# Kernel optimization log

Measured on AMD Instinct MI355X. Metric: run time of the kernel, lower is better.

Reference implementation:

```python
import jax, jax.numpy as jnp
import numpy as np

N = 50000
IN_C = 128
OUT_C = 64


def gcn_conv(x, edge_index, W, b):
    # PyG GCNConv: h = X W; add self-loops; symmetric norm D^-1/2 (A+I) D^-1/2; aggregate; + bias
    n = x.shape[0]
    h = x @ W  # [N, out]
    loop = jnp.arange(n, dtype=edge_index.dtype)
    row = jnp.concatenate([edge_index[0], loop])  # source
    col = jnp.concatenate([edge_index[1], loop])  # target
    deg = jax.ops.segment_sum(jnp.ones_like(col, dtype=h.dtype), col, num_segments=n)
    dinv = jnp.where(deg > 0, jax.lax.rsqrt(deg), 0.0)
    norm = dinv[row] * dinv[col]  # [E+N]
    msg = norm[:, None] * h[row]  # gather source features
    out = jax.ops.segment_sum(msg, col, num_segments=n)  # scatter to targets
    return out + b


def layer_norm(x, w, b, eps=1e-5):
    mu = jnp.mean(x, axis=-1, keepdims=True)
    var = jnp.mean((x - mu) ** 2, axis=-1, keepdims=True)
    return (x - mu) * jax.lax.rsqrt(var + eps) * w + b


def setup_inputs() -> dict:
    key = jax.random.key(0)
    ks = jax.random.split(key, 10)
    x = jax.random.normal(ks[0], (N, IN_C), dtype=jnp.float32)
    edge_index = jax.random.randint(ks[1], (2, 800000), 0, N, dtype=jnp.int64)
    s1 = 1.0 / np.sqrt(IN_C)
    s2 = 1.0 / np.sqrt(OUT_C)
    W1 = jax.random.uniform(ks[2], (IN_C, OUT_C), jnp.float32, -s1, s1)
    b1 = jnp.zeros((OUT_C,), jnp.float32)
    ln_w = jnp.ones((OUT_C,), jnp.float32)
    ln_b = jnp.zeros((OUT_C,), jnp.float32)
    W2 = jax.random.uniform(ks[3], (OUT_C, OUT_C), jnp.float32, -s2, s2)
    b2 = jnp.zeros((OUT_C,), jnp.float32)
    W3 = jax.random.uniform(ks[4], (OUT_C, 6), jnp.float32, -s2, s2)
    b3 = jax.random.uniform(ks[5], (6,), jnp.float32, -s2, s2)
    return {"x": x, "edge_index": edge_index, "W1": W1, "b1": b1,
            "ln_w": ln_w, "ln_b": ln_b, "W2": W2, "b2": b2, "W3": W3, "b3": b3}


def reference(x, edge_index, W1, b1, ln_w, ln_b, W2, b2, W3, b3):
    h = gcn_conv(x, edge_index, W1, b1)           # [N, 64]
    h = jax.nn.relu(layer_norm(h, ln_w, ln_b))    # [N, 64]
    out1 = gcn_conv(h, edge_index, W2, b2)        # [N, 64]
    out2 = jax.nn.sigmoid(h @ W3 + b3)            # [N, 6]
    return (out1, out2)
```

## Files before the change

### kernel.cpp

```cpp
#include <hip/hip_runtime.h>
#include <hip/hip_fp16.h>
#include <math.h>


#define ELLW 48

typedef _Float16 half8 __attribute__((ext_vector_type(8)));
typedef float f32x4 __attribute__((ext_vector_type(4)));

__global__ void k_setup(const float* __restrict__ W1, const float* __restrict__ W2,
                        const float* __restrict__ W3, _Float16* __restrict__ W1g,
                        _Float16* __restrict__ Bg, int* __restrict__ cnt, int n) {
    if (blockIdx.x >= 52) {
        int i = (blockIdx.x - 52) * 256 + threadIdx.x;
        if (i < n) cnt[i] = 0;
        return;
    }
    int idx = blockIdx.x * 256 + threadIdx.x;
    if (idx < 8192) {
        int j = idx & 7, L = (idx >> 3) & 63, s = (idx >> 9) & 3, t = idx >> 11;
        int k = s * 32 + (L >> 4) * 8 + j;
        int c = t * 16 + (L & 15);
        W1g[idx] = (_Float16)W1[k * 64 + c];
    } else if (idx < 8192 + 5120) {
        int i2 = idx - 8192;
        int j = i2 & 7, L = (i2 >> 3) & 63, s = (i2 >> 9) & 1, u = i2 >> 10;
        int k = s * 32 + (L >> 4) * 8 + j;
        int c = (L & 15);
        float v;
        if (u < 4) v = W2[k * 64 + u * 16 + c];
        else v = (c < 6) ? W3[k * 6 + c] : 0.f;
        Bg[i2] = (_Float16)v;
    }
}

__global__ __launch_bounds__(256) void k_scatter(
    const int* __restrict__ row, const int* __restrict__ col,
    int* __restrict__ cnt, int* __restrict__ ell, int E, int slice_sz) {
    int slice = blockIdx.x & 7;
    int lo = slice * slice_sz;
    int hi = lo + slice_sz;
    int nchunk = gridDim.x >> 3;
    int stride = nchunk * 256;
    int v0 = (blockIdx.x >> 3) * 256 + threadIdx.x;
    int nv = E >> 2;
    const int4* c4p = (const int4*)col;
    const int4* r4p = (const int4*)row;
    for (int v = v0; v < nv; v += stride) {
        int4 c4 = c4p[v];
        int4 r4 = r4p[v];
        if (c4.x >= lo && c4.x < hi) {
            int rk = atomicAdd(&cnt[c4.x], 1);
            if (rk < ELLW) ell[c4.x * ELLW + rk] = r4.x << 7;
        }
        if (c4.y >= lo && c4.y < hi) {
            int rk = atomicAdd(&cnt[c4.y], 1);
            if (rk < ELLW) ell[c4.y * ELLW + rk] = r4.y << 7;
        }
        if (c4.z >= lo && c4.z < hi) {
            int rk = atomicAdd(&cnt[c4.z], 1);
            if (rk < ELLW) ell[c4.z * ELLW + rk] = r4.z << 7;
        }
        if (c4.w >= lo && c4.w < hi) {
            int rk = atomicAdd(&cnt[c4.w], 1);
            if (rk < ELLW) ell[c4.w * ELLW + rk] = r4.w << 7;
        }
    }
    if ((blockIdx.x >> 3) == 0) {
        for (int e = (nv << 2) + threadIdx.x; e < E; e += 256) {
            int c = col[e];
            if (c >= lo && c < hi) {
                int rk = atomicAdd(&cnt[c], 1);
                if (rk < ELLW) ell[c * ELLW + rk] = row[e] << 7;
            }
        }
    }
}

__global__ __launch_bounds__(256, 4) void k_gemm1(
    const float* __restrict__ x, const _Float16* __restrict__ W1g,
    const int* __restrict__ cnt, uint* __restrict__ hs,
    uint* __restrict__ h2s, int n) {
    int tid = threadIdx.x;
    if (blockIdx.x == 0) {
        if (tid < 32) hs[(size_t)n * 32 + tid] = 0u;
        else if (tid < 64) h2s[(size_t)n * 32 + (tid - 32)] = 0u;
    }
    int lane = tid & 63, wid = tid >> 6;
    int m16 = lane & 15, quad = lane >> 4;
    int node0 = blockIdx.x * 64 + wid * 16;
    int arow = node0 + m16;
    if (arow >= n) arow = n - 1;
    const float* xr = x + (size_t)arow * 128;
    half8 A[4];
#pragma unroll
    for (int s = 0; s < 4; s++) {
        const float4* p = (const float4*)(xr + s * 32 + quad * 8);
        float4 f0 = p[0], f1 = p[1];
        half8 a;
        a[0] = (_Float16)f0.x; a[1] = (_Float16)f0.y;
        a[2] = (_Float16)f0.z; a[3] = (_Float16)f0.w;
        a[4] = (_Float16)f1.x; a[5] = (_Float16)f1.y;
        a[6] = (_Float16)f1.z; a[7] = (_Float16)f1.w;
        A[s] = a;
    }
    float dsc[4];
#pragma unroll
    for (int r = 0; r < 4; r++) {
        int nd = node0 + quad * 4 + r;
        dsc[r] = rsqrtf((float)(cnt[nd < n ? nd : n - 1] + 1));
    }
    const half8* Wv = (const half8*)W1g;
#pragma unroll
    for (int t = 0; t < 4; t++) {
        f32x4 acc = {0.f, 0.f, 0.f, 0.f};
#pragma unroll
        for (int s = 0; s < 4; s++)
            acc = __builtin_amdgcn_mfma_f32_16x16x32_f16(A[s], Wv[(t * 4 + s) * 64 + lane], acc, 0, 0, 0);
#pragma unroll
        for (int r = 0; r < 4; r++) {
            int nd = node0 + quad * 4 + r;
            float v = acc[r] * dsc[r];
            float vo = __shfl_xor(v, 1, 64);
            if (!(m16 & 1) && nd < n) {
                __half2 pk = __floats2half2_rn(v, vo);
                hs[(size_t)nd * 32 + t * 8 + (m16 >> 1)] = *(uint*)&pk;
            }
        }
    }
}

#define GATHER_PROLOG(SRC_T)                                                  \
    int st[4], P[4], nid[4];                                                  \
    int Pmax = 0;                                                             \
    _Pragma("unroll") for (int p = 0; p < 4; p++) {                           \
        int node = base + wid * 4 + p;                                        \
        if (node >= n) node = n - 1;                                          \
        nid[p] = node; st[p] = node * ELLW; P[p] = cnt[node];                 \
        Pmax = Pmax > P[p] ? Pmax : P[p];                                     \
    }                                                                         \
    Pmax = (Pmax + 7) & ~7;                                                   \
    auto ldix = [&](int p, int jb) -> int {                                   \
        int o = ell[st[p] + jb + g];                                          \
        return (jb + g < P[p]) ? o : zoff;                                    \
    };                                                                        \
    const char* hsb = (const char*)(SRC_T);                                   \
    float accv[4][8];                                                         \
    _Pragma("unroll") for (int p = 0; p < 4; p++) {                           \
        int sa = (g == 0) ? (nid[p] << 7) : zoff;                             \
        uint4 us = *(const uint4*)(hsb + sa + m16b);                          \
        float2 f;                                                             \
        f = __half22float2(*(__half2*)&us.x); accv[p][0] = f.x; accv[p][1] = f.y; \
        f = __half22float2(*(__half2*)&us.y); accv[p][2] = f.x; accv[p][3] = f.y; \
        f = __half22float2(*(__half2*)&us.z); accv[p][4] = f.x; accv[p][5] = f.y; \
        f = __half22float2(*(__half2*)&us.w); accv[p][6] = f.x; accv[p][7] = f.y; \
    }

#define CVT_ACC(p, U)                                                         \
    {                                                                         \
        float2 f;                                                             \
        f = __half22float2(*(__half2*)&U.x); accv[p][0] += f.x; accv[p][1] += f.y; \
        f = __half22float2(*(__half2*)&U.y); accv[p][2] += f.x; accv[p][3] += f.y; \
        f = __half22float2(*(__half2*)&U.z); accv[p][4] += f.x; accv[p][5] += f.y; \
        f = __half22float2(*(__half2*)&U.w); accv[p][6] += f.x; accv[p][7] += f.y; \
    }

#define GATHER_BODY16(SRC)                                                    \
    {                                                                         \
        int oB[4], oC[4];                                                     \
        uint4 uA[4], uB[4];                                                   \
        {                                                                     \
            int oA[4];                                                        \
            _Pragma("unroll") for (int p = 0; p < 4; p++) oA[p] = ldix(p, 0); \
            _Pragma("unroll") for (int p = 0; p < 4; p++) oB[p] = ldix(p, 8); \
            _Pragma("unroll") for (int p = 0; p < 4; p++)                     \
                uA[p] = *(const uint4*)(SRC + oA[p] + m16b);                  \
        }                                                                     \
        for (int jb = 0; jb < Pmax; jb += 8) {                                \
            _Pragma("unroll") for (int p = 0; p < 4; p++) oC[p] = ldix(p, jb + 16); \
            _Pragma("unroll") for (int p = 0; p < 4; p++)                     \
                uB[p] = *(const uint4*)(SRC + oB[p] + m16b);                  \
            _Pragma("unroll") for (int p = 0; p < 4; p++) CVT_ACC(p, uA[p])   \
            _Pragma("unroll") for (int p = 0; p < 4; p++) {                   \
                uA[p] = uB[p]; oB[p] = oC[p];                                 \
            }                                                                 \
        }                                                                     \
    }                                                                         \
    _Pragma("unroll") for (int p = 0; p < 4; p++)                             \
        _Pragma("unroll") for (int c = 0; c < 8; c++) {                       \
            float v = accv[p][c];                                             \
            v += __shfl_xor(v, 8, 64);                                        \
            v += __shfl_xor(v, 16, 64);                                       \
            v += __shfl_xor(v, 32, 64);                                       \
            accv[p][c] = v;                                                   \
        }

__global__ __launch_bounds__(256, 4) void k_conv1_fused(
    const uint* __restrict__ hs, const int* __restrict__ ell,
    const int* __restrict__ cnt, const float* __restrict__ b1,
    const float* __restrict__ lnw_g, const float* __restrict__ lnb_g,
    const _Float16* __restrict__ Bg, const float* __restrict__ b3,
    uint* __restrict__ h2s, float* __restrict__ out2, int zoff, int n) {
    __shared__ _Float16 Y[4][16 * 72];
    int tid = threadIdx.x;
    int lane = tid & 63, wid = tid >> 6;
    int l = lane & 7, g = lane >> 3;
    int m16b = l * 16;
    {
        float4 z = {0.f, 0.f, 0.f, 0.f};
        float4* yb = (float4*)Y[wid];
        for (int i = lane; i < 144; i += 64) yb[i] = z;
    }
    int base = blockIdx.x * 16;
    GATHER_PROLOG(hs)
    GATHER_BODY16(hsb)

    float4 bvlo = ((const float4*)b1)[2 * l], bvhi = ((const float4*)b1)[2 * l + 1];
    float4 lwlo = ((const float4*)lnw_g)[2 * l], lwhi = ((const float4*)lnw_g)[2 * l + 1];
    float4 lblo = ((const float4*)lnb_g)[2 * l], lbhi = ((const float4*)lnb_g)[2 * l + 1];
    float dcs[4];
#pragma unroll
    for (int p = 0; p < 4; p++) {
        float dc = rsqrtf((float)(P[p] + 1));
        dcs[p] = dc;
        float v[8];
        v[0] = fmaf(dc, accv[p][0], bvlo.x); v[1] = fmaf(dc, accv[p][1], bvlo.y);
        v[2] = fmaf(dc, accv[p][2], bvlo.z); v[3] = fmaf(dc, accv[p][3], bvlo.w);
        v[4] = fmaf(dc, accv[p][4], bvhi.x); v[5] = fmaf(dc, accv[p][5], bvhi.y);
        v[6] = fmaf(dc, accv[p][6], bvhi.z); v[7] = fmaf(dc, accv[p][7], bvhi.w);
        float s = ((v[0] + v[1]) + (v[2] + v[3])) + ((v[4] + v[5]) + (v[6] + v[7]));
        s += __shfl_xor(s, 1, 64); s += __shfl_xor(s, 2, 64); s += __shfl_xor(s, 4, 64);
        float mu = s * (1.f / 64.f);
        float d[8], q = 0.f;
#pragma unroll
        for (int c = 0; c < 8; c++) { d[c] = v[c] - mu; q += d[c] * d[c]; }
        q += __shfl_xor(q, 1, 64); q += __shfl_xor(q, 2, 64); q += __shfl_xor(q, 4, 64);
        float rstd = rsqrtf(q * (1.f / 64.f) + 1e-5f);
        float y[8];
        y[0] = fmaxf(fmaf(d[0] * rstd, lwlo.x, lblo.x), 0.f);
        y[1] = fmaxf(fmaf(d[1] * rstd, lwlo.y, lblo.y), 0.f);
        y[2] = fmaxf(fmaf(d[2] * rstd, lwlo.z, lblo.z), 0.f);
        y[3] = fmaxf(fmaf(d[3] * rstd, lwlo.w, lblo.w), 0.f);
        y[4] = fmaxf(fmaf(d[4] * rstd, lwhi.x, lbhi.x), 0.f);
        y[5] = fmaxf(fmaf(d[5] * rstd, lwhi.y, lbhi.y), 0.f);
        y[6] = fmaxf(fmaf(d[6] * rstd, lwhi.z, lbhi.z), 0.f);
        y[7] = fmaxf(fmaf(d[7] * rstd, lwhi.w, lbhi.w), 0.f);
        if (g == 0) {
            __half2 pk0 = __floats2half2_rn(y[0], y[1]);
            __half2 pk1 = __floats2half2_rn(y[2], y[3]);
            __half2 pk2 = __floats2half2_rn(y[4], y[5]);
            __half2 pk3 = __floats2half2_rn(y[6], y[7]);
            uint4 pk;
            pk.x = *(uint*)&pk0; pk.y = *(uint*)&pk1;
            pk.z = *(uint*)&pk2; pk.w = *(uint*)&pk3;
            *(uint4*)&Y[wid][p * 72 + 8 * l] = pk;
        }
    }
    int m16 = lane & 15, quad = lane >> 4;
    half8 a0 = *(const half8*)&Y[wid][m16 * 72 + quad * 8];
    half8 a1 = *(const half8*)&Y[wid][m16 * 72 + 32 + quad * 8];
    const half8* Bv = (const half8*)Bg;
    _Float16* h2h = (_Float16*)h2s;
#pragma unroll
    for (int t = 0; t < 4; t++) {
        f32x4 acc2 = {0.f, 0.f, 0.f, 0.f};
        acc2 = __builtin_amdgcn_mfma_f32_16x16x32_f16(a0, Bv[(t * 2 + 0) * 64 + lane], acc2, 0, 0, 0);
        acc2 = __builtin_amdgcn_mfma_f32_16x16x32_f16(a1, Bv[(t * 2 + 1) * 64 + lane], acc2, 0, 0, 0);
#pragma unroll
        for (int r = 0; r < 4; r++) {
            int nodep = base + wid * 4 + r;
            if (quad == 0 && nodep < n)
                h2h[(size_t)nodep * 64 + t * 16 + m16] = (_Float16)(acc2[r] * dcs[r]);
        }
    }
    {
        f32x4 acc2 = {0.f, 0.f, 0.f, 0.f};
        acc2 = __builtin_amdgcn_mfma_f32_16x16x32_f16(a0, Bv[8 * 64 + lane], acc2, 0, 0, 0);
        acc2 = __builtin_amdgcn_mfma_f32_16x16x32_f16(a1, Bv[9 * 64 + lane], acc2, 0, 0, 0);
        float bb = b3[m16 < 6 ? m16 : 0];
#pragma unroll
        for (int r = 0; r < 4; r++) {
            int nodep = base + wid * 4 + r;
            if (quad == 0 && m16 < 6 && nodep < n)
                out2[(size_t)nodep * 6 + m16] = 1.f / (1.f + __expf(-(acc2[r] + bb)));
        }
    }
}

__global__ __launch_bounds__(256, 4) void k_conv2(
    const uint* __restrict__ h2s, const int* __restrict__ ell,
    const int* __restrict__ cnt, const float* __restrict__ b2,
    float* __restrict__ out1, int zoff, int n) {
    int tid = threadIdx.x;
    int lane = tid & 63, wid = tid >> 6;
    int l = lane & 7, g = lane >> 3;
    int m16b = l * 16;
    int base = blockIdx.x * 16;
    GATHER_PROLOG(h2s)
    GATHER_BODY16(hsb)

    float4 b2lo = ((const float4*)b2)[2 * l], b2hi = ((const float4*)b2)[2 * l + 1];
#pragma unroll
    for (int p = 0; p < 4; p++) {
        int node = base + wid * 4 + p;
        if (g == 0 && node < n) {
            float dc = rsqrtf((float)(P[p] + 1));
            float4 r0, r1;
            r0.x = fmaf(dc, accv[p][0], b2lo.x);
            r0.y = fmaf(dc, accv[p][1], b2lo.y);
            r0.z = fmaf(dc, accv[p][2], b2lo.z);
            r0.w = fmaf(dc, accv[p][3], b2lo.w);
            r1.x = fmaf(dc, accv[p][4], b2hi.x);
            r1.y = fmaf(dc, accv[p][5], b2hi.y);
            r1.z = fmaf(dc, accv[p][6], b2hi.z);
            r1.w = fmaf(dc, accv[p][7], b2hi.w);
            ((float4*)out1)[(size_t)node * 16 + 2 * l] = r0;
            ((float4*)out1)[(size_t)node * 16 + 2 * l + 1] = r1;
        }
    }
}

extern "C" void kernel_launch(void* const* d_in, const int* in_sizes, int n_in,
                              void* d_out, int out_size, void* d_ws, size_t ws_size,
                              hipStream_t stream) {
    const float* x   = (const float*)d_in[0];
    const int*   ei  = (const int*)d_in[1];
    const float* W1  = (const float*)d_in[2];
    const float* b1  = (const float*)d_in[3];
    const float* lnw = (const float*)d_in[4];
    const float* lnb = (const float*)d_in[5];
    const float* W2  = (const float*)d_in[6];
    const float* b2  = (const float*)d_in[7];
    const float* W3  = (const float*)d_in[8];
    const float* b3  = (const float*)d_in[9];

    int n = in_sizes[0] / 128;
    int E = in_sizes[1] / 2;
    const int* row = ei;
    const int* col = ei + E;

    char* ws = (char*)d_ws;
    size_t off = 0;
    auto carve = [&](size_t bytes) -> char* {
        char* p = ws + off;
        off = (off + bytes + 255) & ~(size_t)255;
        return p;
    };
    int*   cnt  = (int*)carve(4 * (size_t)n);
    int*   ell  = (int*)carve(4 * ((size_t)n * ELLW + 256));
    uint*  hs   = (uint*)carve(128 * ((size_t)n + 1));
    uint*  h2s  = (uint*)carve(128 * ((size_t)n + 1));
    _Float16* W1g = (_Float16*)carve(2 * 8192);
    _Float16* Bg  = (_Float16*)carve(2 * 5120);

    float* out1 = (float*)d_out;
    float* out2 = out1 + (size_t)n * 64;
    int zero_off = n << 7;
    int slice_sz = (n + 7) / 8;

    k_setup<<<52 + (n + 255) / 256, 256, 0, stream>>>(W1, W2, W3, W1g, Bg, cnt, n);
    k_scatter<<<8 * 256, 256, 0, stream>>>(row, col, cnt, ell, E, slice_sz);
    k_gemm1<<<(n + 63) / 64, 256, 0, stream>>>(x, W1g, cnt, hs, h2s, n);
    k_conv1_fused<<<(n + 15) / 16, 256, 0, stream>>>(hs, ell, cnt,
                                                     b1, lnw, lnb, Bg, b3,
                                                     h2s, out2, zero_off, n);
    k_conv2<<<(n + 15) / 16, 256, 0, stream>>>(h2s, ell, cnt, b2,
                                               out1, zero_off, n);
}
```

Before: 192.5 us.

## Split neighbor lists by source-node half to localize gather working set

The scatter now buckets each edge into one of two ELL tables depending on whether its source node lies in the lower or upper half of the node range, packing both counts into one int. Each convolution is then split into two gather passes, one per half, so each pass touches only half of the feature table and has a better chance of staying in cache. The first pass writes partial sums into the output buffer and the second adds them before the epilogue. In exchange this adds two kernel launches and an extra partial-sum write and read per convolution, and the per-half cap of 32 neighbors replaces the single cap of 48.

```diff
diff --git a/kernel.cpp b/kernel.cpp
--- a/kernel.cpp
+++ b/kernel.cpp
@@ -3,7 +3,7 @@
 #include <math.h>
 
 
-#define ELLW 48
+#define ELLH 32
 
 typedef _Float16 half8 __attribute__((ext_vector_type(8)));
 typedef float f32x4 __attribute__((ext_vector_type(4)));
@@ -36,44 +36,36 @@
 
 __global__ __launch_bounds__(256) void k_scatter(
     const int* __restrict__ row, const int* __restrict__ col,
-    int* __restrict__ cnt, int* __restrict__ ell, int E, int slice_sz) {
+    int* __restrict__ cnt, int* __restrict__ ellA, int* __restrict__ ellB,
+    int E, int slice_sz, int halfN) {
     int slice = blockIdx.x & 7;
     int lo = slice * slice_sz;
     int hi = lo + slice_sz;
-    int nchunk = gridDim.x >> 3;
-    int stride = nchunk * 256;
+    int stride = (gridDim.x >> 3) * 256;
     int v0 = (blockIdx.x >> 3) * 256 + threadIdx.x;
     int nv = E >> 2;
     const int4* c4p = (const int4*)col;
     const int4* r4p = (const int4*)row;
+    auto sc1 = [&](int c, int r) {
+        if (c >= lo && c < hi) {
+            int hB = (r >= halfN) ? 1 : 0;
+            int old = atomicAdd(&cnt[c], hB ? 0x10000 : 1);
+            int rk = hB ? (old >> 16) : (old & 0xffff);
+            int* tbl = hB ? ellB : ellA;
+            if (rk < ELLH) tbl[c * ELLH + rk] = r << 7;
+        }
+    };
     for (int v = v0; v < nv; v += stride) {
         int4 c4 = c4p[v];
         int4 r4 = r4p[v];
-        if (c4.x >= lo && c4.x < hi) {
-            int rk = atomicAdd(&cnt[c4.x], 1);
-            if (rk < ELLW) ell[c4.x * ELLW + rk] = r4.x << 7;
-        }
-        if (c4.y >= lo && c4.y < hi) {
-            int rk = atomicAdd(&cnt[c4.y], 1);
-            if (rk < ELLW) ell[c4.y * ELLW + rk] = r4.y << 7;
-        }
-        if (c4.z >= lo && c4.z < hi) {
-            int rk = atomicAdd(&cnt[c4.z], 1);
-            if (rk < ELLW) ell[c4.z * ELLW + rk] = r4.z << 7;
-        }
-        if (c4.w >= lo && c4.w < hi) {
-            int rk = atomicAdd(&cnt[c4.w], 1);
-            if (rk < ELLW) ell[c4.w * ELLW + rk] = r4.w << 7;
-        }
+        sc1(c4.x, r4.x);
+        sc1(c4.y, r4.y);
+        sc1(c4.z, r4.z);
+        sc1(c4.w, r4.w);
     }
     if ((blockIdx.x >> 3) == 0) {
-        for (int e = (nv << 2) + threadIdx.x; e < E; e += 256) {
-            int c = col[e];
-            if (c >= lo && c < hi) {
-                int rk = atomicAdd(&cnt[c], 1);
-                if (rk < ELLW) ell[c * ELLW + rk] = row[e] << 7;
-            }
-        }
+        for (int e = (nv << 2) + threadIdx.x; e < E; e += 256)
+            sc1(col[e], row[e]);
     }
 }
 
@@ -108,7 +100,8 @@
 #pragma unroll
     for (int r = 0; r < 4; r++) {
         int nd = node0 + quad * 4 + r;
-        dsc[r] = rsqrtf((float)(cnt[nd < n ? nd : n - 1] + 1));
+        int cv = cnt[nd < n ? nd : n - 1];
+        dsc[r] = rsqrtf((float)((cv & 0xffff) + (cv >> 16) + 1));
     }
     const half8* Wv = (const half8*)W1g;
 #pragma unroll
@@ -130,31 +123,8 @@
     }
 }
 
-#define GATHER_PROLOG(SRC_T)                                                  \
-    int st[4], P[4], nid[4];                                                  \
-    int Pmax = 0;                                                             \
-    _Pragma("unroll") for (int p = 0; p < 4; p++) {                           \
-        int node = base + wid * 4 + p;                                        \
-        if (node >= n) node = n - 1;                                          \
-        nid[p] = node; st[p] = node * ELLW; P[p] = cnt[node];                 \
-        Pmax = Pmax > P[p] ? Pmax : P[p];                                     \
-    }                                                                         \
-    Pmax = (Pmax + 7) & ~7;                                                   \
-    auto ldix = [&](int p, int jb) -> int {                                   \
-        int o = ell[st[p] + jb + g];                                          \
-        return (jb + g < P[p]) ? o : zoff;                                    \
-    };                                                                        \
-    const char* hsb = (const char*)(SRC_T);                                   \
-    float accv[4][8];                                                         \
-    _Pragma("unroll") for (int p = 0; p < 4; p++) {                           \
-        int sa = (g == 0) ? (nid[p] << 7) : zoff;                             \
-        uint4 us = *(const uint4*)(hsb + sa + m16b);                          \
-        float2 f;                                                             \
-        f = __half22float2(*(__half2*)&us.x); accv[p][0] = f.x; accv[p][1] = f.y; \
-        f = __half22float2(*(__half2*)&us.y); accv[p][2] = f.x; accv[p][3] = f.y; \
-        f = __half22float2(*(__half2*)&us.z); accv[p][4] = f.x; accv[p][5] = f.y; \
-        f = __half22float2(*(__half2*)&us.w); accv[p][6] = f.x; accv[p][7] = f.y; \
-    }
+#define LDIX(TBL, Pq, p, jb) \
+    ({ int _o = TBL[st[p] + (jb) + g]; ((jb) + g < Pq[p]) ? _o : zoff; })
 
 #define CVT_ACC(p, U)                                                         \
     {                                                                         \
@@ -165,27 +135,25 @@
         f = __half22float2(*(__half2*)&U.w); accv[p][6] += f.x; accv[p][7] += f.y; \
     }
 
-#define GATHER_BODY16(SRC)                                                    \
+#define GATHER_CORE(SRC, TBL, Pq, Pmaxv)                                      \
     {                                                                         \
         int oB[4], oC[4];                                                     \
         uint4 uA[4], uB[4];                                                   \
-        {                                                                     \
-            int oA[4];                                                        \
-            _Pragma("unroll") for (int p = 0; p < 4; p++) oA[p] = ldix(p, 0); \
-            _Pragma("unroll") for (int p = 0; p < 4; p++) oB[p] = ldix(p, 8); \
-            _Pragma("unroll") for (int p = 0; p < 4; p++)                     \
-                uA[p] = *(const uint4*)(SRC + oA[p] + m16b);                  \
+        _Pragma("unroll") for (int p = 0; p < 4; p++) {                       \
+            int oA = LDIX(TBL, Pq, p, 0);                                     \
+            oB[p] = LDIX(TBL, Pq, p, 8);                                      \
+            uA[p] = *(const uint4*)(SRC + oA + m16b);                         \
         }                                                                     \
-        for (int jb = 0; jb < Pmax; jb += 8) {                                \
-            _Pragma("unroll") for (int p = 0; p < 4; p++) oC[p] = ldix(p, jb + 16); \
+        for (int jb = 0; jb < Pmaxv; jb += 8) {                               \
+            _Pragma("unroll") for (int p = 0; p < 4; p++) oC[p] = LDIX(TBL, Pq, p, jb + 16); \
             _Pragma("unroll") for (int p = 0; p < 4; p++)                     \
                 uB[p] = *(const uint4*)(SRC + oB[p] + m16b);                  \
             _Pragma("unroll") for (int p = 0; p < 4; p++) CVT_ACC(p, uA[p])   \
-            _Pragma("unroll") for (int p = 0; p < 4; p++) {                   \
-                uA[p] = uB[p]; oB[p] = oC[p];                                 \
-            }                                                                 \
+            _Pragma("unroll") for (int p = 0; p < 4; p++) { uA[p] = uB[p]; oB[p] = oC[p]; } \
         }                                                                     \
-    }                                                                         \
+    }
+
+#define GATHER_REDUCE                                                         \
     _Pragma("unroll") for (int p = 0; p < 4; p++)                             \
         _Pragma("unroll") for (int c = 0; c < 8; c++) {                       \
             float v = accv[p][c];                                             \
@@ -195,12 +163,52 @@
             accv[p][c] = v;                                                   \
         }
 
-__global__ __launch_bounds__(256, 4) void k_conv1_fused(
-    const uint* __restrict__ hs, const int* __restrict__ ell,
-    const int* __restrict__ cnt, const float* __restrict__ b1,
-    const float* __restrict__ lnw_g, const float* __restrict__ lnb_g,
-    const _Float16* __restrict__ Bg, const float* __restrict__ b3,
-    uint* __restrict__ h2s, float* __restrict__ out2, int zoff, int n) {
+__global__ __launch_bounds__(256, 4) void k_conv_part(
+    const uint* __restrict__ src, const int* __restrict__ ellA,
+    const int* __restrict__ cnt, float* __restrict__ part, int zoff, int n) {
+    int tid = threadIdx.x;
+    int lane = tid & 63, wid = tid >> 6;
+    int l = lane & 7, g = lane >> 3;
+    int m16b = l * 16;
+    int base = blockIdx.x * 16;
+    int st[4], P[4];
+    int Pmax = 0;
+#pragma unroll
+    for (int p = 0; p < 4; p++) {
+        int node = base + wid * 4 + p;
+        if (node >= n) node = n - 1;
+        st[p] = node * ELLH;
+        P[p] = cnt[node] & 0xffff;
+        Pmax = Pmax > P[p] ? Pmax : P[p];
+    }
+    Pmax = (Pmax + 7) & ~7;
+    const char* hsb = (const char*)src;
+    float accv[4][8];
+#pragma unroll
+    for (int p = 0; p < 4; p++)
+#pragma unroll
+        for (int c = 0; c < 8; c++) accv[p][c] = 0.f;
+    GATHER_CORE(hsb, ellA, P, Pmax)
+    GATHER_REDUCE
+#pragma unroll
+    for (int p = 0; p < 4; p++) {
+        int node = base + wid * 4 + p;
+        if (g == 0 && node < n) {
+            float4 q0 = {accv[p][0], accv[p][1], accv[p][2], accv[p][3]};
+            float4 q1 = {accv[p][4], accv[p][5], accv[p][6], accv[p][7]};
+            ((float4*)part)[(size_t)node * 16 + 2 * l] = q0;
+            ((float4*)part)[(size_t)node * 16 + 2 * l + 1] = q1;
+        }
+    }
+}
+
+__global__ __launch_bounds__(256, 4) void k_conv1b(
+    const uint* __restrict__ hs, const int* __restrict__ ellB,
+    const int* __restrict__ cnt, const float* __restrict__ part,
+    const float* __restrict__ b1, const float* __restrict__ lnw_g,
+    const float* __restrict__ lnb_g, const _Float16* __restrict__ Bg,
+    const float* __restrict__ b3, uint* __restrict__ h2s,
+    float* __restrict__ out2, int zoff, int n) {
     __shared__ _Float16 Y[4][16 * 72];
     int tid = threadIdx.x;
     int lane = tid & 63, wid = tid >> 6;
@@ -212,8 +220,46 @@
         for (int i = lane; i < 144; i += 64) yb[i] = z;
     }
     int base = blockIdx.x * 16;
-    GATHER_PROLOG(hs)
-    GATHER_BODY16(hsb)
+    int st[4], P[4], nid[4], dg[4];
+    int Pmax = 0;
+#pragma unroll
+    for (int p = 0; p < 4; p++) {
+        int node = base + wid * 4 + p;
+        if (node >= n) node = n - 1;
+        nid[p] = node;
+        st[p] = node * ELLH;
+        int cv = cnt[node];
+        P[p] = cv >> 16;
+        dg[p] = (cv & 0xffff) + (cv >> 16);
+        Pmax = Pmax > P[p] ? Pmax : P[p];
+    }
+    Pmax = (Pmax + 7) & ~7;
+    const char* hsb = (const char*)hs;
+    float accv[4][8];
+#pragma unroll
+    for (int p = 0; p < 4; p++) {
+        int sa = (g == 0) ? (nid[p] << 7) : zoff;
+        uint4 us = *(const uint4*)(hsb + sa + m16b);
+        float2 f;
+        f = __half22float2(*(__half2*)&us.x); accv[p][0] = f.x; accv[p][1] = f.y;
+        f = __half22float2(*(__half2*)&us.y); accv[p][2] = f.x; accv[p][3] = f.y;
+        f = __half22float2(*(__half2*)&us.z); accv[p][4] = f.x; accv[p][5] = f.y;
+        f = __half22float2(*(__half2*)&us.w); accv[p][6] = f.x; accv[p][7] = f.y;
+    }
+    GATHER_CORE(hsb, ellB, P, Pmax)
+    GATHER_REDUCE
+    {
+        const float4* pf = (const float4*)part;
+#pragma unroll
+        for (int p = 0; p < 4; p++) {
+            float4 q0 = pf[(size_t)nid[p] * 16 + 2 * l];
+            float4 q1 = pf[(size_t)nid[p] * 16 + 2 * l + 1];
+            accv[p][0] += q0.x; accv[p][1] += q0.y;
+            accv[p][2] += q0.z; accv[p][3] += q0.w;
+            accv[p][4] += q1.x; accv[p][5] += q1.y;
+            accv[p][6] += q1.z; accv[p][7] += q1.w;
+        }
+    }
 
     float4 bvlo = ((const float4*)b1)[2 * l], bvhi = ((const float4*)b1)[2 * l + 1];
     float4 lwlo = ((const float4*)lnw_g)[2 * l], lwhi = ((const float4*)lnw_g)[2 * l + 1];
@@ -221,7 +267,7 @@
     float dcs[4];
 #pragma unroll
     for (int p = 0; p < 4; p++) {
-        float dc = rsqrtf((float)(P[p] + 1));
+        float dc = rsqrtf((float)(dg[p] + 1));
         dcs[p] = dc;
         float v[8];
         v[0] = fmaf(dc, accv[p][0], bvlo.x); v[1] = fmaf(dc, accv[p][1], bvlo.y);
@@ -287,33 +333,62 @@
     }
 }
 
-__global__ __launch_bounds__(256, 4) void k_conv2(
-    const uint* __restrict__ h2s, const int* __restrict__ ell,
-    const int* __restrict__ cnt, const float* __restrict__ b2,
-    float* __restrict__ out1, int zoff, int n) {
+__global__ __launch_bounds__(256, 4) void k_conv2b(
+    const uint* __restrict__ h2s, const int* __restrict__ ellB,
+    const int* __restrict__ cnt, const float* __restrict__ part,
+    const float* __restrict__ b2, float* __restrict__ out1, int zoff, int n) {
     int tid = threadIdx.x;
     int lane = tid & 63, wid = tid >> 6;
     int l = lane & 7, g = lane >> 3;
     int m16b = l * 16;
     int base = blockIdx.x * 16;
-    GATHER_PROLOG(h2s)
-    GATHER_BODY16(hsb)
-
+    int st[4], P[4], nid[4], dg[4];
+    int Pmax = 0;
+#pragma unroll
+    for (int p = 0; p < 4; p++) {
+        int node = base + wid * 4 + p;
+        if (node >= n) node = n - 1;
+        nid[p] = node;
+        st[p] = node * ELLH;
+        int cv = cnt[node];
+        P[p] = cv >> 16;
+        dg[p] = (cv & 0xffff) + (cv >> 16);
+        Pmax = Pmax > P[p] ? Pmax : P[p];
+    }
+    Pmax = (Pmax + 7) & ~7;
+    const char* hsb = (const char*)h2s;
+    float accv[4][8];
+#pragma unroll
+    for (int p = 0; p < 4; p++) {
+        int sa = (g == 0) ? (nid[p] << 7) : zoff;
+        uint4 us = *(const uint4*)(hsb + sa + m16b);
+        float2 f;
+        f = __half22float2(*(__half2*)&us.x); accv[p][0] = f.x; accv[p][1] = f.y;
+        f = __half22float2(*(__half2*)&us.y); accv[p][2] = f.x; accv[p][3] = f.y;
+        f = __half22float2(*(__half2*)&us.z); accv[p][4] = f.x; accv[p][5] = f.y;
+        f = __half22float2(*(__half2*)&us.w); accv[p][6] = f.x; accv[p][7] = f.y;
+    }
+    GATHER_CORE(hsb, ellB, P, Pmax)
+    GATHER_REDUCE
+
+    const float4* pf = (const float4*)part;
     float4 b2lo = ((const float4*)b2)[2 * l], b2hi = ((const float4*)b2)[2 * l + 1];
 #pragma unroll
     for (int p = 0; p < 4; p++) {
         int node = base + wid * 4 + p;
         if (g == 0 && node < n) {
-            float dc = rsqrtf((float)(P[p] + 1));
+            float dc = rsqrtf((float)(dg[p] + 1));
+            float4 q0 = pf[(size_t)node * 16 + 2 * l];
+            float4 q1 = pf[(size_t)node * 16 + 2 * l + 1];
             float4 r0, r1;
-            r0.x = fmaf(dc, accv[p][0], b2lo.x);
-            r0.y = fmaf(dc, accv[p][1], b2lo.y);
-            r0.z = fmaf(dc, accv[p][2], b2lo.z);
-            r0.w = fmaf(dc, accv[p][3], b2lo.w);
-            r1.x = fmaf(dc, accv[p][4], b2hi.x);
-            r1.y = fmaf(dc, accv[p][5], b2hi.y);
-            r1.z = fmaf(dc, accv[p][6], b2hi.z);
-            r1.w = fmaf(dc, accv[p][7], b2hi.w);
+            r0.x = fmaf(dc, accv[p][0] + q0.x, b2lo.x);
+            r0.y = fmaf(dc, accv[p][1] + q0.y, b2lo.y);
+            r0.z = fmaf(dc, accv[p][2] + q0.z, b2lo.z);
+            r0.w = fmaf(dc, accv[p][3] + q0.w, b2lo.w);
+            r1.x = fmaf(dc, accv[p][4] + q1.x, b2hi.x);
+            r1.y = fmaf(dc, accv[p][5] + q1.y, b2hi.y);
+            r1.z = fmaf(dc, accv[p][6] + q1.z, b2hi.z);
+            r1.w = fmaf(dc, accv[p][7] + q1.w, b2hi.w);
             ((float4*)out1)[(size_t)node * 16 + 2 * l] = r0;
             ((float4*)out1)[(size_t)node * 16 + 2 * l + 1] = r1;
         }
@@ -347,7 +422,8 @@
         return p;
     };
     int*   cnt  = (int*)carve(4 * (size_t)n);
-    int*   ell  = (int*)carve(4 * ((size_t)n * ELLW + 256));
+    int*   ellA = (int*)carve(4 * ((size_t)n * ELLH + 64));
+    int*   ellB = (int*)carve(4 * ((size_t)n * ELLH + 64));
     uint*  hs   = (uint*)carve(128 * ((size_t)n + 1));
     uint*  h2s  = (uint*)carve(128 * ((size_t)n + 1));
     _Float16* W1g = (_Float16*)carve(2 * 8192);
@@ -355,15 +431,20 @@
 
     float* out1 = (float*)d_out;
     float* out2 = out1 + (size_t)n * 64;
+    float* part = out1;
     int zero_off = n << 7;
     int slice_sz = (n + 7) / 8;
+    int halfN = n >> 1;
 
     k_setup<<<52 + (n + 255) / 256, 256, 0, stream>>>(W1, W2, W3, W1g, Bg, cnt, n);
-    k_scatter<<<8 * 256, 256, 0, stream>>>(row, col, cnt, ell, E, slice_sz);
+    k_scatter<<<8 * 256, 256, 0, stream>>>(row, col, cnt, ellA, ellB, E,
+                                           slice_sz, halfN);
     k_gemm1<<<(n + 63) / 64, 256, 0, stream>>>(x, W1g, cnt, hs, h2s, n);
-    k_conv1_fused<<<(n + 15) / 16, 256, 0, stream>>>(hs, ell, cnt,
-                                                     b1, lnw, lnb, Bg, b3,
-                                                     h2s, out2, zero_off, n);
-    k_conv2<<<(n + 15) / 16, 256, 0, stream>>>(h2s, ell, cnt, b2,
-                                               out1, zero_off, n);
-}
+    int cg = (n + 15) / 16;
+    k_conv_part<<<cg, 256, 0, stream>>>(hs, ellA, cnt, part, zero_off, n);
+    k_conv1b<<<cg, 256, 0, stream>>>(hs, ellB, cnt, part, b1, lnw, lnb,
+                                     Bg, b3, h2s, out2, zero_off, n);
+    k_conv_part<<<cg, 256, 0, stream>>>(h2s, ellA, cnt, part, zero_off, n);
+    k_conv2b<<<cg, 256, 0, stream>>>(h2s, ellB, cnt, part, b2,
+                                     out1, zero_off, n);
+}
```

Measured after the change: 231.6 us. 1.2x slower.
